# Optimization experiments

Hardware: AMD Instinct MI355X
Metric: run time of the kernel (lower is better)

The kernel has to match this reference:

```python
import jax, jax.numpy as jnp
import numpy as np

N_USERS = 50000
N0, N1, N2 = 200000, 50000, 12500
E0, E1, E2 = 1600000, 400000, 100000
B = 128
NUMP, TWEET, CATP, DES = 6, 768, 2, 768
IN_DIM, HID = 128, 128
SLOPE = 0.01  # LeakyReLU default


def setup_inputs() -> dict:
    key = jax.random.key(0)
    ks = iter(jax.random.split(key, 32))
    f32 = jnp.float32
    nrm = lambda s, sc=0.05: jax.random.normal(next(ks), s, f32) * sc
    inp = {}
    inp['x_raw'] = jax.random.normal(next(ks), (N_USERS, NUMP + TWEET + CATP + DES), f32)
    inp['W_des'] = nrm((DES, IN_DIM // 4)); inp['b_des'] = jnp.zeros((IN_DIM // 4,), f32)
    inp['W_tweet'] = nrm((TWEET, IN_DIM // 4)); inp['b_tweet'] = jnp.zeros((IN_DIM // 4,), f32)
    inp['W_num'] = nrm((NUMP, IN_DIM // 4)); inp['b_num'] = jnp.zeros((IN_DIM // 4,), f32)
    inp['W_cat'] = nrm((CATP, IN_DIM // 4)); inp['b_cat'] = jnp.zeros((IN_DIM // 4,), f32)
    inp['W_in'] = nrm((IN_DIM, HID)); inp['b_in'] = jnp.zeros((HID,), f32)
    inp['prelu_a'] = jnp.full((HID,), 0.25, f32)
    inp['W_conv'] = nrm((3, HID, HID)); inp['b_conv'] = jnp.zeros((3, HID), f32)
    inp['Wc1'] = nrm((3 * HID, HID)); inp['bc1'] = jnp.zeros((HID,), f32)
    inp['Wc2'] = nrm((HID, HID)); inp['bc2'] = jnp.zeros((HID,), f32)
    ri = lambda n, hi: jax.random.randint(next(ks), (n,), 0, hi, jnp.int32)
    inp['nodelist'] = ri(N0, N_USERS)
    inp['e0'] = jnp.stack([ri(E0, N0), ri(E0, N0)])
    inp['e1'] = jnp.stack([ri(E1, N1), ri(E1, N1)])
    inp['e2'] = jnp.stack([ri(E2, N2), ri(E2, N2)])
    inp['parent1'] = ri(N0, N1)   # coarsening assignment layer0 -> layer1
    inp['parent2'] = ri(N1, N2)   # layer1 -> layer2
    inp['batch1'] = jnp.sort(ri(N1, B))
    inp['batch2'] = jnp.sort(ri(N2, B))
    return inp


def _leaky(x):
    return jnp.where(x > 0, x, SLOPE * x)


def _gcn(h, ei, W, b, n):
    # GCNConv: lin -> sym-normalized add-aggregation with self-loops -> +bias
    h = h @ W
    loop = jnp.arange(n, dtype=ei.dtype)
    src = jnp.concatenate([ei[0], loop])
    dst = jnp.concatenate([ei[1], loop])
    deg = jax.ops.segment_sum(jnp.ones(dst.shape, h.dtype), dst, num_segments=n)
    dinv = jnp.where(deg > 0, jax.lax.rsqrt(deg), 0.0)
    msg = h[src] * (dinv[src] * dinv[dst])[:, None]
    return jax.ops.segment_sum(msg, dst, num_segments=n) + b


def reference(x_raw, W_des, b_des, W_tweet, b_tweet, W_num, b_num, W_cat, b_cat,
              W_in, b_in, prelu_a, W_conv, b_conv, Wc1, bc1, Wc2, bc2,
              nodelist, e0, e1, e2, parent1, parent2, batch1, batch2):
    # FeatureEncoder (twibot-20 slicing order: num_prop | tweet | cat_prop | des)
    n = _leaky(x_raw[:, :NUMP] @ W_num + b_num)
    t = _leaky(x_raw[:, NUMP:NUMP + TWEET] @ W_tweet + b_tweet)
    c = _leaky(x_raw[:, NUMP + TWEET:NUMP + TWEET + CATP] @ W_cat + b_cat)
    d = _leaky(x_raw[:, NUMP + TWEET + CATP:] @ W_des + b_des)
    h = jnp.concatenate([d, t, n, c], axis=1) @ W_in + b_in
    enc = jnp.where(h > 0, h, prelu_a * h)  # PReLU

    x = enc[nodelist]  # [N0, HID] gather per batched nodelists
    edges = [e0, e1, e2]
    sizes = [N0, N1, N2]
    parents = [parent1, parent2]
    nxt = [N1, N2]
    xs = []
    for i in range(3):
        x = jax.nn.relu(_gcn(x, edges[i], W_conv[i], b_conv[i], sizes[i]))
        if i < 2:  # SEPooling: pure scatter-add onto parent nodes (nn unused in its forward)
            x = jax.nn.relu(jax.ops.segment_sum(x, parents[i], num_segments=nxt[i]))
        xs.append(x)
    pooled = jnp.concatenate([
        jax.ops.segment_sum(xs[0], batch1, num_segments=B),
        jax.ops.segment_sum(xs[1], batch2, num_segments=B),
        jax.ops.segment_sum(xs[2], batch2, num_segments=B),
    ], axis=1)  # global sum pool, batch at layer min(i+1, tree_depth-1)
    z = jax.nn.relu(pooled @ Wc1 + bc1)  # dropout inactive (eval)
    return z @ Wc2 + bc2
```

## Files before the change

### kernel.cpp

```cpp
#include <hip/hip_runtime.h>

#define N_USERS 50000
#define NN0 200000
#define NN1 50000
#define NN2 12500
#define EE0 1600000
#define EE1 400000
#define EE2 100000

#define ENC_BLOCKS 782
#define CNT_BLOCKS 2295
#define GM2_BLOCKS 1563


__global__ __launch_bounds__(256) void k_enc_count(
    const float* __restrict__ xr,
    const float* __restrict__ Wd, const float* __restrict__ bd,
    const float* __restrict__ Wt, const float* __restrict__ bt,
    const float* __restrict__ Wn, const float* __restrict__ bn,
    const float* __restrict__ Wc, const float* __restrict__ bc,
    float* __restrict__ h128,
    const int* __restrict__ d0, const int* __restrict__ d1, const int* __restrict__ d2,
    const int* __restrict__ p1, const int* __restrict__ p2,
    int* __restrict__ degs, int* __restrict__ ranks)
{
    __shared__ float XsB[4368];
    __shared__ float Ws[32][68];
    __shared__ float xnc[64][8];
    __shared__ float Wl[8][64];

    if (blockIdx.x >= ENC_BLOCKS) {
        int t0 = (blockIdx.x - ENC_BLOCKS) * 256 + threadIdx.x;
        if (t0 >= 587500) return;
        #pragma unroll
        for (int k = 0; k < 4; k++) {
            int gid = t0 + k * 587500;
            int idx;
            if (gid < 1600000)      idx = d0[gid];
            else if (gid < 2000000) idx = 200704 + d1[gid - 1600000];
            else if (gid < 2100000) idx = 250880 + d2[gid - 2000000];
            else if (gid < 2300000) idx = 264192 + p1[gid - 2100000];
            else                    idx = 314368 + p2[gid - 2300000];
            ranks[gid] = atomicAdd(&degs[idx], 1);
        }
        return;
    }

    int t = threadIdx.x;
    int lane = t & 63, wv = t >> 6;
    int cg = t & 15, rg = t >> 4;
    int base = blockIdx.x * 64;

    if (t < 64) {
        int row = base + t;
        if (row < N_USERS) {
            const float* xp = xr + (size_t)row * 1544;
            float4 a = *(const float4*)xp;
            float2 b2 = *(const float2*)(xp + 4);
            float2 c2 = *(const float2*)(xp + 774);
            xnc[t][0] = a.x; xnc[t][1] = a.y; xnc[t][2] = a.z; xnc[t][3] = a.w;
            xnc[t][4] = b2.x; xnc[t][5] = b2.y; xnc[t][6] = c2.x; xnc[t][7] = c2.y;
        } else {
            #pragma unroll
            for (int k = 0; k < 8; k++) xnc[t][k] = 0.f;
        }
    } else if (t >= 192) {
        int l = t - 192;
        #pragma unroll
        for (int k = 0; k < 8; k++) {
            float w = 0.f;
            if (l < 32) { if (k < 6) w = Wn[k * 32 + l]; }
            else        { if (k >= 6) w = Wc[(k - 6) * 32 + (l - 32)]; }
            Wl[k][l] = w;
        }
    }

    int srow = (lane & 15) + wv * 16;
    int grow = base + srow;
    bool vrow = grow < N_USERS;
    const float* xrow = xr + (size_t)grow * 1544;

    float acc[4][4];
    #pragma unroll
    for (int r = 0; r < 4; r++)
        #pragma unroll
        for (int c = 0; c < 4; c++) acc[r][c] = 0.f;

    for (int kc = 0; kc < 768; kc += 32) {
        __syncthreads();
        #pragma unroll
        for (int h = 0; h < 2; h++) {
            int q = (lane >> 4) + h * 4;
            float4 vd = {0.f, 0.f, 0.f, 0.f};
            float2 va = {0.f, 0.f}, vb = {0.f, 0.f};
            if (vrow) {
                const float* xp = xrow + kc + q * 4;
                vd = *(const float4*)(xp + 776);
                va = *(const float2*)(xp + 6);
                vb = *(const float2*)(xp + 8);
            }
            int k0 = q * 4;
            XsB[(k0 + 0) * 68 + srow] = vd.x;
            XsB[(k0 + 1) * 68 + srow] = vd.y;
            XsB[(k0 + 2) * 68 + srow] = vd.z;
            XsB[(k0 + 3) * 68 + srow] = vd.w;
            XsB[2192 + (k0 + 0) * 68 + srow] = va.x;
            XsB[2192 + (k0 + 1) * 68 + srow] = va.y;
            XsB[2192 + (k0 + 2) * 68 + srow] = vb.x;
            XsB[2192 + (k0 + 3) * 68 + srow] = vb.y;
        }
        #pragma unroll
        for (int h = 0; h < 2; h++) {
            int fi = t + h * 256;
            int k = fi >> 4, c4 = (fi & 15) * 4;
            float4 w = (c4 < 32) ? *(const float4*)(Wd + (size_t)(kc + k) * 32 + c4)
                                 : *(const float4*)(Wt + (size_t)(kc + k) * 32 + (c4 - 32));
            *(float4*)&Ws[k][c4] = w;
        }
        __syncthreads();

        const float* Xp = (cg < 8) ? XsB : (XsB + 2192);
        #pragma unroll 8
        for (int k = 0; k < 32; k++) {
            float4 xv = *(const float4*)(Xp + k * 68 + rg * 4);
            float4 wv2 = *(const float4*)&Ws[k][cg * 4];
            acc[0][0] = fmaf(xv.x, wv2.x, acc[0][0]);
            acc[0][1] = fmaf(xv.x, wv2.y, acc[0][1]);
            acc[0][2] = fmaf(xv.x, wv2.z, acc[0][2]);
            acc[0][3] = fmaf(xv.x, wv2.w, acc[0][3]);
            acc[1][0] = fmaf(xv.y, wv2.x, acc[1][0]);
            acc[1][1] = fmaf(xv.y, wv2.y, acc[1][1]);
            acc[1][2] = fmaf(xv.y, wv2.z, acc[1][2]);
            acc[1][3] = fmaf(xv.y, wv2.w, acc[1][3]);
            acc[2][0] = fmaf(xv.z, wv2.x, acc[2][0]);
            acc[2][1] = fmaf(xv.z, wv2.y, acc[2][1]);
            acc[2][2] = fmaf(xv.z, wv2.z, acc[2][2]);
            acc[2][3] = fmaf(xv.z, wv2.w, acc[2][3]);
            acc[3][0] = fmaf(xv.w, wv2.x, acc[3][0]);
            acc[3][1] = fmaf(xv.w, wv2.y, acc[3][1]);
            acc[3][2] = fmaf(xv.w, wv2.z, acc[3][2]);
            acc[3][3] = fmaf(xv.w, wv2.w, acc[3][3]);
        }
    }

    float bh[4], bl[4], wlv[8][4];
    #pragma unroll
    for (int c = 0; c < 4; c++) {
        int j = cg * 4 + c;
        bh[c] = (j < 32) ? bd[j] : bt[j - 32];
        bl[c] = (j < 32) ? bn[j] : bc[j - 32];
        #pragma unroll
        for (int k = 0; k < 8; k++) wlv[k][c] = Wl[k][j];
    }
    #pragma unroll
    for (int r = 0; r < 4; r++) {
        int lr = rg * 4 + r;
        int row = base + lr;
        if (row >= N_USERS) break;
        float4 hv;
        float* ph = &hv.x;
        #pragma unroll
        for (int c = 0; c < 4; c++) {
            float v = acc[r][c] + bh[c];
            ph[c] = v > 0.f ? v : 0.01f * v;
        }
        *(float4*)(h128 + (size_t)row * 128 + cg * 4) = hv;
        float4 lv;
        float* pl = &lv.x;
        #pragma unroll
        for (int c = 0; c < 4; c++) {
            float v = bl[c];
            #pragma unroll
            for (int k = 0; k < 8; k++) v = fmaf(xnc[lr][k], wlv[k][c], v);
            pl[c] = v > 0.f ? v : 0.01f * v;
        }
        *(float4*)(h128 + (size_t)row * 128 + 64 + cg * 4) = lv;
    }
}

__global__ __launch_bounds__(256) void k_gemm2_scatter(
    const float* __restrict__ X, const float* __restrict__ W1,
    const float* __restrict__ b1, const float* __restrict__ pa,
    const float* __restrict__ W2, float* __restrict__ OUT, int n,
    const int* __restrict__ s0, const int* __restrict__ d0,
    const int* __restrict__ s1, const int* __restrict__ d1,
    const int* __restrict__ s2, const int* __restrict__ d2,
    const int* __restrict__ p1, const int* __restrict__ p2,
    const int* __restrict__ nl, const float* __restrict__ dinvs,
    const int* __restrict__ rowsts, const int* __restrict__ ranks,
    int* __restrict__ elists, float* __restrict__ edw)
{
    __shared__ float Xs[32][132];
    __shared__ float Wsh[32][132];

    if (blockIdx.x >= GM2_BLOCKS) {
        int t0 = (blockIdx.x - GM2_BLOCKS) * 256 + threadIdx.x;
        if (t0 >= 587500) return;
        #pragma unroll
        for (int k = 0; k < 4; k++) {
            int gid = t0 + k * 587500;
            if (gid < 1600000) {
                int s = s0[gid];
                int p = rowsts[d0[gid]] + ranks[gid];
                elists[p] = nl[s];
                edw[p] = dinvs[s];
            } else if (gid < 2000000) {
                int i = gid - 1600000;
                int s = s1[i];
                int p = rowsts[200704 + d1[i]] + ranks[gid];
                elists[1600000 + p] = s;
                edw[1600000 + p] = dinvs[200704 + s];
            } else if (gid < 2100000) {
                int i = gid - 2000000;
                int s = s2[i];
                int p = rowsts[250880 + d2[i]] + ranks[gid];
                elists[2000000 + p] = s;
                edw[2000000 + p] = dinvs[250880 + s];
            } else if (gid < 2300000) {
                int i = gid - 2100000;
                int p = rowsts[264192 + p1[i]] + ranks[gid];
                elists[2100000 + p] = i;
            } else {
                int i = gid - 2300000;
                int p = rowsts[314368 + p2[i]] + ranks[gid];
                elists[2300000 + p] = i;
            }
        }
        return;
    }

    int t = threadIdx.x;
    int cg = t & 31, rg = t >> 5;
    int base = blockIdx.x * 32;

    #pragma unroll
    for (int h = 0; h < 4; h++) {
        int fi = t + h * 256;
        int row = fi >> 5, q = fi & 31;
        float4 v = {0.f, 0.f, 0.f, 0.f};
        if (base + row < n) v = *(const float4*)(X + (size_t)(base + row) * 128 + q * 4);
        *(float4*)&Xs[row][q * 4] = v;
    }

    float acc[4][4];
    #pragma unroll
    for (int r = 0; r < 4; r++)
        #pragma unroll
        for (int c = 0; c < 4; c++) acc[r][c] = 0.f;

    for (int kc = 0; kc < 128; kc += 32) {
        __syncthreads();
        #pragma unroll
        for (int h = 0; h < 4; h++) {
            int fi = t + h * 256;
            int k = fi >> 5, q = fi & 31;
            *(float4*)&Wsh[k][q * 4] = *(const float4*)(W1 + (size_t)(kc + k) * 128 + q * 4);
        }
        __syncthreads();
        #pragma unroll
        for (int k4 = 0; k4 < 8; k4++) {
            int k = k4 * 4;
            float4 w0 = *(const float4*)&Wsh[k + 0][cg * 4];
            float4 w1 = *(const float4*)&Wsh[k + 1][cg * 4];
            float4 w2 = *(const float4*)&Wsh[k + 2][cg * 4];
            float4 w3 = *(const float4*)&Wsh[k + 3][cg * 4];
            #pragma unroll
            for (int r = 0; r < 4; r++) {
                float4 xv = *(const float4*)&Xs[rg * 4 + r][kc + k];
                acc[r][0] = fmaf(xv.w, w3.x, fmaf(xv.z, w2.x, fmaf(xv.y, w1.x, fmaf(xv.x, w0.x, acc[r][0]))));
                acc[r][1] = fmaf(xv.w, w3.y, fmaf(xv.z, w2.y, fmaf(xv.y, w1.y, fmaf(xv.x, w0.y, acc[r][1]))));
                acc[r][2] = fmaf(xv.w, w3.z, fmaf(xv.z, w2.z, fmaf(xv.y, w1.z, fmaf(xv.x, w0.z, acc[r][2]))));
                acc[r][3] = fmaf(xv.w, w3.w, fmaf(xv.z, w2.w, fmaf(xv.y, w1.w, fmaf(xv.x, w0.w, acc[r][3]))));
            }
        }
    }

    float4 bv = *(const float4*)(b1 + cg * 4);
    float4 pv = *(const float4*)(pa + cg * 4);
    __syncthreads();
    #pragma unroll
    for (int r = 0; r < 4; r++) {
        float v0 = acc[r][0] + bv.x; v0 = v0 > 0.f ? v0 : pv.x * v0;
        float v1 = acc[r][1] + bv.y; v1 = v1 > 0.f ? v1 : pv.y * v1;
        float v2 = acc[r][2] + bv.z; v2 = v2 > 0.f ? v2 : pv.z * v2;
        float v3 = acc[r][3] + bv.w; v3 = v3 > 0.f ? v3 : pv.w * v3;
        Xs[rg * 4 + r][cg * 4 + 0] = v0;
        Xs[rg * 4 + r][cg * 4 + 1] = v1;
        Xs[rg * 4 + r][cg * 4 + 2] = v2;
        Xs[rg * 4 + r][cg * 4 + 3] = v3;
        acc[r][0] = 0.f; acc[r][1] = 0.f; acc[r][2] = 0.f; acc[r][3] = 0.f;
    }

    for (int kc = 0; kc < 128; kc += 32) {
        __syncthreads();
        #pragma unroll
        for (int h = 0; h < 4; h++) {
            int fi = t + h * 256;
            int k = fi >> 5, q = fi & 31;
            *(float4*)&Wsh[k][q * 4] = *(const float4*)(W2 + (size_t)(kc + k) * 128 + q * 4);
        }
        __syncthreads();
        #pragma unroll
        for (int k4 = 0; k4 < 8; k4++) {
            int k = k4 * 4;
            float4 w0 = *(const float4*)&Wsh[k + 0][cg * 4];
            float4 w1 = *(const float4*)&Wsh[k + 1][cg * 4];
            float4 w2 = *(const float4*)&Wsh[k + 2][cg * 4];
            float4 w3 = *(const float4*)&Wsh[k + 3][cg * 4];
            #pragma unroll
            for (int r = 0; r < 4; r++) {
                float4 xv = *(const float4*)&Xs[rg * 4 + r][kc + k];
                acc[r][0] = fmaf(xv.w, w3.x, fmaf(xv.z, w2.x, fmaf(xv.y, w1.x, fmaf(xv.x, w0.x, acc[r][0]))));
                acc[r][1] = fmaf(xv.w, w3.y, fmaf(xv.z, w2.y, fmaf(xv.y, w1.y, fmaf(xv.x, w0.y, acc[r][1]))));
                acc[r][2] = fmaf(xv.w, w3.z, fmaf(xv.z, w2.z, fmaf(xv.y, w1.z, fmaf(xv.x, w0.z, acc[r][2]))));
                acc[r][3] = fmaf(xv.w, w3.w, fmaf(xv.z, w2.w, fmaf(xv.y, w1.w, fmaf(xv.x, w0.w, acc[r][3]))));
            }
        }
    }

    #pragma unroll
    for (int r = 0; r < 4; r++) {
        int row = base + rg * 4 + r;
        if (row >= n) break;
        float4 v;
        v.x = acc[r][0]; v.y = acc[r][1]; v.z = acc[r][2]; v.w = acc[r][3];
        *(float4*)(OUT + (size_t)row * 128 + cg * 4) = v;
    }
}

__global__ __launch_bounds__(256) void k_gemmT(
    const float* X, const float* __restrict__ W, float* OUT, int n)
{
    __shared__ float Xs[32][132];
    __shared__ float Ws[32][132];
    int t = threadIdx.x;
    int cg = t & 31, rg = t >> 5;
    int base = blockIdx.x * 32;

    #pragma unroll
    for (int h = 0; h < 4; h++) {
        int fi = t + h * 256;
        int row = fi >> 5, q = fi & 31;
        float4 v = {0.f, 0.f, 0.f, 0.f};
        if (base + row < n) v = *(const float4*)(X + (size_t)(base + row) * 128 + q * 4);
        *(float4*)&Xs[row][q * 4] = v;
    }

    float acc[4][4];
    #pragma unroll
    for (int r = 0; r < 4; r++)
        #pragma unroll
        for (int c = 0; c < 4; c++) acc[r][c] = 0.f;

    for (int kc = 0; kc < 128; kc += 32) {
        __syncthreads();
        #pragma unroll
        for (int h = 0; h < 4; h++) {
            int fi = t + h * 256;
            int k = fi >> 5, q = fi & 31;
            *(float4*)&Ws[k][q * 4] = *(const float4*)(W + (size_t)(kc + k) * 128 + q * 4);
        }
        __syncthreads();
        #pragma unroll
        for (int k4 = 0; k4 < 8; k4++) {
            int k = k4 * 4;
            float4 w0 = *(const float4*)&Ws[k + 0][cg * 4];
            float4 w1 = *(const float4*)&Ws[k + 1][cg * 4];
            float4 w2 = *(const float4*)&Ws[k + 2][cg * 4];
            float4 w3 = *(const float4*)&Ws[k + 3][cg * 4];
            #pragma unroll
            for (int r = 0; r < 4; r++) {
                float4 xv = *(const float4*)&Xs[rg * 4 + r][kc + k];
                acc[r][0] = fmaf(xv.w, w3.x, fmaf(xv.z, w2.x, fmaf(xv.y, w1.x, fmaf(xv.x, w0.x, acc[r][0]))));
                acc[r][1] = fmaf(xv.w, w3.y, fmaf(xv.z, w2.y, fmaf(xv.y, w1.y, fmaf(xv.x, w0.y, acc[r][1]))));
                acc[r][2] = fmaf(xv.w, w3.z, fmaf(xv.z, w2.z, fmaf(xv.y, w1.z, fmaf(xv.x, w0.z, acc[r][2]))));
                acc[r][3] = fmaf(xv.w, w3.w, fmaf(xv.z, w2.w, fmaf(xv.y, w1.w, fmaf(xv.x, w0.w, acc[r][3]))));
            }
        }
    }

    #pragma unroll
    for (int r = 0; r < 4; r++) {
        int row = base + rg * 4 + r;
        if (row >= n) break;
        float4 v;
        v.x = acc[r][0]; v.y = acc[r][1]; v.z = acc[r][2]; v.w = acc[r][3];
        *(float4*)(OUT + (size_t)row * 128 + cg * 4) = v;
    }
}

__device__ __forceinline__ void seg_of_scanblk(int b, int& doff, int& bsoff, int& lb) {
    if (b < 196)      { doff = 0;      bsoff = 0;   lb = b; }
    else if (b < 245) { doff = 200704; bsoff = 196; lb = b - 196; }
    else if (b < 258) { doff = 250880; bsoff = 245; lb = b - 245; }
    else if (b < 307) { doff = 264192; bsoff = 258; lb = b - 258; }
    else              { doff = 314368; bsoff = 307; lb = b - 307; }
}

__global__ __launch_bounds__(256) void k_scan_all(
    const int* __restrict__ degs, int* __restrict__ rowsts, int* __restrict__ bsums)
{
    __shared__ int sh[256];
    int doff, bsoff, lb;
    seg_of_scanblk(blockIdx.x, doff, bsoff, lb);
    int t = threadIdx.x;
    int base = doff + lb * 1024 + t * 4;
    int v[4], s = 0;
    #pragma unroll
    for (int k = 0; k < 4; k++) { v[k] = degs[base + k]; s += v[k]; }
    sh[t] = s;
    __syncthreads();
    for (int off = 1; off < 256; off <<= 1) {
        int x = 0;
        if (t >= off) x = sh[t - off];
        __syncthreads();
        if (t >= off) sh[t] += x;
        __syncthreads();
    }
    int ex = sh[t] - s;
    if (t == 255) bsums[bsoff + lb] = sh[255];
    #pragma unroll
    for (int k = 0; k < 4; k++) { rowsts[base + k] = ex; ex += v[k]; }
}

__global__ __launch_bounds__(256) void k_scanadd_all(
    int* __restrict__ rowsts, const int* __restrict__ bsums,
    const int* __restrict__ degs, float* __restrict__ dinvs)
{
    __shared__ int sh[256];
    int doff, bsoff, lb;
    seg_of_scanblk(blockIdx.x, doff, bsoff, lb);
    int t = threadIdx.x;
    sh[t] = (t < lb) ? bsums[bsoff + t] : 0;
    __syncthreads();
    #pragma unroll
    for (int off = 128; off >= 1; off >>= 1) {
        if (t < off) sh[t] += sh[t + off];
        __syncthreads();
    }
    int add = sh[0];
    int base = doff + lb * 1024 + t * 4;
    bool dodinv = (doff <= 250880);
    #pragma unroll
    for (int k = 0; k < 4; k++) {
        int i = base + k;
        rowsts[i] += add;
        if (dodinv) dinvs[i] = rsqrtf((float)degs[i] + 1.0f);
    }
}

__global__ __launch_bounds__(256) void k_gatherU_perm(
    const float* __restrict__ U, const int* __restrict__ nl,
    const int* __restrict__ rowst, const int* __restrict__ elist,
    const float* __restrict__ edw, const float* __restrict__ dinv,
    const float* __restrict__ bias, const int* __restrict__ perm,
    float* __restrict__ out, int n)
{
    size_t gid = (size_t)blockIdx.x * 256 + threadIdx.x;
    int i = (int)(gid >> 5);
    if (i >= n) return;
    int l = (int)(gid & 31);
    int d = perm[i];
    const float4* Uv = (const float4*)U;
    float dd = dinv[d];
    float4 self = Uv[(size_t)nl[d] * 32 + l];
    float4 acc;
    acc.x = self.x * dd; acc.y = self.y * dd; acc.z = self.z * dd; acc.w = self.w * dd;
    int s0 = rowst[d], s1 = rowst[d + 1];
    for (int e = s0; e < s1; ++e) {
        int srow = elist[e];
        float w = edw[e];
        float4 v = Uv[(size_t)srow * 32 + l];
        acc.x = fmaf(v.x, w, acc.x);
        acc.y = fmaf(v.y, w, acc.y);
        acc.z = fmaf(v.z, w, acc.z);
        acc.w = fmaf(v.w, w, acc.w);
    }
    const float4 b = ((const float4*)bias)[l];
    float4 y;
    y.x = fmaxf(fmaf(acc.x, dd, b.x), 0.f);
    y.y = fmaxf(fmaf(acc.y, dd, b.y), 0.f);
    y.z = fmaxf(fmaf(acc.z, dd, b.z), 0.f);
    y.w = fmaxf(fmaf(acc.w, dd, b.w), 0.f);
    ((float4*)out)[(size_t)i * 32 + l] = y;
}

__global__ __launch_bounds__(256) void k_gather_perm(
    const float* __restrict__ h, const int* __restrict__ rowst,
    const int* __restrict__ elist, const float* __restrict__ edw,
    const float* __restrict__ dinv, const float* __restrict__ bias,
    const int* __restrict__ perm, float* __restrict__ out, int n)
{
    size_t gid = (size_t)blockIdx.x * 256 + threadIdx.x;
    int i = (int)(gid >> 5);
    if (i >= n) return;
    int l = (int)(gid & 31);
    int d = perm ? perm[i] : i;
    const float4* hv = (const float4*)h;
    float dd = dinv[d];
    float4 self = hv[(size_t)d * 32 + l];
    float4 acc;
    acc.x = self.x * dd; acc.y = self.y * dd; acc.z = self.z * dd; acc.w = self.w * dd;
    int s0 = rowst[d], s1 = rowst[d + 1];
    for (int e = s0; e < s1; ++e) {
        int srow = elist[e];
        float w = edw[e];
        float4 v = hv[(size_t)srow * 32 + l];
        acc.x = fmaf(v.x, w, acc.x);
        acc.y = fmaf(v.y, w, acc.y);
        acc.z = fmaf(v.z, w, acc.z);
        acc.w = fmaf(v.w, w, acc.w);
    }
    const float4 b = ((const float4*)bias)[l];
    float4 y;
    y.x = fmaxf(fmaf(acc.x, dd, b.x), 0.f);
    y.y = fmaxf(fmaf(acc.y, dd, b.y), 0.f);
    y.z = fmaxf(fmaf(acc.z, dd, b.z), 0.f);
    y.w = fmaxf(fmaf(acc.w, dd, b.w), 0.f);
    ((float4*)out)[(size_t)i * 32 + l] = y;
}

__global__ __launch_bounds__(256) void k_poolseq(
    const float* __restrict__ Yp, const int* __restrict__ prowst,
    float* __restrict__ out, int np)
{
    size_t gid = (size_t)blockIdx.x * 256 + threadIdx.x;
    int p = (int)(gid >> 5);
    if (p >= np) return;
    int l = (int)(gid & 31);
    const float4* yv = (const float4*)Yp;
    float4 acc = {0.f, 0.f, 0.f, 0.f};
    int c0 = prowst[p], c1 = prowst[p + 1];
    for (int c = c0; c < c1; ++c) {
        float4 v = yv[(size_t)c * 32 + l];
        acc.x += v.x; acc.y += v.y; acc.z += v.z; acc.w += v.w;
    }
    float4 y;
    y.x = fmaxf(acc.x, 0.f); y.y = fmaxf(acc.y, 0.f);
    y.z = fmaxf(acc.z, 0.f); y.w = fmaxf(acc.w, 0.f);
    ((float4*)out)[(size_t)p * 32 + l] = y;
}

__global__ __launch_bounds__(128) void k_bpool_all(
    const float* __restrict__ X1, const float* __restrict__ X2, const float* __restrict__ Y2,
    const int* __restrict__ b1, const int* __restrict__ b2, float* __restrict__ pl)
{
    int b = blockIdx.x;
    const float* src; const int* bidx; int coloff, n, r0;
    if (b < 391)      { src = X1; bidx = b1; coloff = 0;   n = 50000; r0 = b * 128; }
    else if (b < 489) { src = X2; bidx = b2; coloff = 128; n = 12500; r0 = (b - 391) * 128; }
    else              { src = Y2; bidx = b2; coloff = 256; n = 12500; r0 = (b - 489) * 128; }
    if (r0 >= n) return;
    int j = threadIdx.x;
    int r1 = min(r0 + 128, n);
    float acc = 0.f;
    int prev = bidx[r0];
    for (int r = r0; r < r1; ++r) {
        int bb = bidx[r];
        if (bb != prev) {
            unsafeAtomicAdd(&pl[(size_t)prev * 384 + coloff + j], acc);
            acc = 0.f; prev = bb;
        }
        acc += src[(size_t)r * 128 + j];
    }
    unsafeAtomicAdd(&pl[(size_t)prev * 384 + coloff + j], acc);
}

__global__ void k_mlp2(const float* __restrict__ PL,
                       const float* __restrict__ Wc1, const float* __restrict__ bc1,
                       const float* __restrict__ Wc2, const float* __restrict__ bc2,
                       float* __restrict__ out)
{
    __shared__ float as[384];
    __shared__ float zs[128];
    int r = blockIdx.x, j = threadIdx.x;
    as[j] = PL[(size_t)r * 384 + j];
    as[j + 128] = PL[(size_t)r * 384 + 128 + j];
    as[j + 256] = PL[(size_t)r * 384 + 256 + j];
    __syncthreads();
    float acc = bc1[j];
    for (int k = 0; k < 384; k++) acc = fmaf(as[k], Wc1[(size_t)k * 128 + j], acc);
    zs[j] = fmaxf(acc, 0.f);
    __syncthreads();
    float o = bc2[j];
    for (int k = 0; k < 128; k++) o = fmaf(zs[k], Wc2[(size_t)k * 128 + j], o);
    out[(size_t)r * 128 + j] = o;
}

extern "C" void kernel_launch(void* const* d_in, const int* in_sizes, int n_in,
                              void* d_out, int out_size, void* d_ws, size_t ws_size,
                              hipStream_t stream)
{
    const float* x_raw  = (const float*)d_in[0];
    const float* W_des  = (const float*)d_in[1];
    const float* b_des  = (const float*)d_in[2];
    const float* W_twe  = (const float*)d_in[3];
    const float* b_twe  = (const float*)d_in[4];
    const float* W_num  = (const float*)d_in[5];
    const float* b_num  = (const float*)d_in[6];
    const float* W_cat  = (const float*)d_in[7];
    const float* b_cat  = (const float*)d_in[8];
    const float* W_in   = (const float*)d_in[9];
    const float* b_in   = (const float*)d_in[10];
    const float* prelua = (const float*)d_in[11];
    const float* W_conv = (const float*)d_in[12];
    const float* b_conv = (const float*)d_in[13];
    const float* Wc1    = (const float*)d_in[14];
    const float* bc1    = (const float*)d_in[15];
    const float* Wc2    = (const float*)d_in[16];
    const float* bc2    = (const float*)d_in[17];
    const int* nodelist = (const int*)d_in[18];
    const int* e0       = (const int*)d_in[19];
    const int* e1       = (const int*)d_in[20];
    const int* e2       = (const int*)d_in[21];
    const int* parent1  = (const int*)d_in[22];
    const int* parent2  = (const int*)d_in[23];
    const int* batch1   = (const int*)d_in[24];
    const int* batch2   = (const int*)d_in[25];

    float* WS  = (float*)d_ws;
    float* ENC = WS;
    float* U   = WS + 6400000;
    float* H   = WS + 12800000;
    float* Y   = WS + 19200000;
    float* X1  = WS + 44800000;
    float* X2  = WS + 51200000;
    float* PL  = WS + 52800000;
    float* EDW = WS + 52900000;
    int*   DEGS   = (int*)(WS + 55000000);
    int*   ROWSTS = DEGS + 327680;
    float* DINVS  = (float*)(ROWSTS + 327680);
    int*   BSUMS  = (int*)(DINVS + 264192);
    int*   RANKS  = BSUMS + 512;
    int*   ELISTS = RANKS + 2350000;

    hipMemsetAsync(PL, 0, (size_t)128 * 384 * 4, stream);
    hipMemsetAsync(DEGS, 0, (size_t)327680 * 4, stream);

    k_enc_count<<<ENC_BLOCKS + CNT_BLOCKS, 256, 0, stream>>>(
        x_raw, W_des, b_des, W_twe, b_twe, W_num, b_num, W_cat, b_cat, ENC,
        e0 + EE0, e1 + EE1, e2 + EE2, parent1, parent2, DEGS, RANKS);

    k_scan_all<<<320, 256, 0, stream>>>(DEGS, ROWSTS, BSUMS);
    k_scanadd_all<<<320, 256, 0, stream>>>(ROWSTS, BSUMS, DEGS, DINVS);

    k_gemm2_scatter<<<GM2_BLOCKS + CNT_BLOCKS, 256, 0, stream>>>(
        ENC, W_in, b_in, prelua, W_conv, U, N_USERS,
        e0, e0 + EE0, e1, e1 + EE1, e2, e2 + EE2, parent1, parent2,
        nodelist, DINVS, ROWSTS, RANKS, ELISTS, EDW);

    k_gatherU_perm<<<(int)(((size_t)NN0 * 32 + 255) / 256), 256, 0, stream>>>(
        U, nodelist, ROWSTS, ELISTS, EDW, DINVS, b_conv,
        ELISTS + 2100000, Y, NN0);
    k_poolseq<<<(int)(((size_t)NN1 * 32 + 255) / 256), 256, 0, stream>>>(
        Y, ROWSTS + 264192, X1, NN1);

    k_gemmT<<<(NN1 + 31) / 32, 256, 0, stream>>>(X1, W_conv + 16384, H, NN1);
    k_gather_perm<<<(int)(((size_t)NN1 * 32 + 255) / 256), 256, 0, stream>>>(
        H, ROWSTS + 200704, ELISTS + 1600000, EDW + 1600000, DINVS + 200704,
        b_conv + 128, ELISTS + 2300000, Y, NN1);
    k_poolseq<<<(int)(((size_t)NN2 * 32 + 255) / 256), 256, 0, stream>>>(
        Y, ROWSTS + 314368, X2, NN2);

    k_gemmT<<<(NN2 + 31) / 32, 256, 0, stream>>>(X2, W_conv + 32768, H, NN2);
    k_gather_perm<<<(int)(((size_t)NN2 * 32 + 255) / 256), 256, 0, stream>>>(
        H, ROWSTS + 250880, ELISTS + 2000000, EDW + 2000000, DINVS + 250880,
        b_conv + 256, nullptr, Y, NN2);

    k_bpool_all<<<587, 128, 0, stream>>>(X1, X2, Y, batch1, batch2, PL);

    k_mlp2<<<128, 128, 0, stream>>>(PL, Wc1, bc1, Wc2, bc2, (float*)d_out);
}
```

Before: 646.9 us.

## Split encoder K-dimension across two block sets and defer bias/activation to consumer

The encoder GEMM's 768-long reduction is split in half across two sets of blocks, doubling the block count from 782 to 1564 for better occupancy of the MI355X's CUs. Each half writes a partial sum to a separate buffer (enc0 and enc1, with enc1 aliased onto H). The following gemm2 kernel then sums the partials, adds the biases, and applies LeakyReLU while loading its tile. This costs an extra 64-column write and read of partial sums per row, plus a bias staging sync.

```diff
diff --git a/kernel.cpp b/kernel.cpp
--- a/kernel.cpp
+++ b/kernel.cpp
@@ -8,18 +8,17 @@
 #define EE1 400000
 #define EE2 100000
 
-#define ENC_BLOCKS 782
+#define ENC_SPLIT_BLOCKS 782
+#define ENC_TOT 1564
 #define CNT_BLOCKS 2295
 #define GM2_BLOCKS 1563
 
 
 __global__ __launch_bounds__(256) void k_enc_count(
     const float* __restrict__ xr,
-    const float* __restrict__ Wd, const float* __restrict__ bd,
-    const float* __restrict__ Wt, const float* __restrict__ bt,
-    const float* __restrict__ Wn, const float* __restrict__ bn,
-    const float* __restrict__ Wc, const float* __restrict__ bc,
-    float* __restrict__ h128,
+    const float* __restrict__ Wd, const float* __restrict__ Wt,
+    const float* __restrict__ Wn, const float* __restrict__ Wc,
+    float* __restrict__ enc0, float* __restrict__ enc1,
     const int* __restrict__ d0, const int* __restrict__ d1, const int* __restrict__ d2,
     const int* __restrict__ p1, const int* __restrict__ p2,
     int* __restrict__ degs, int* __restrict__ ranks)
@@ -29,8 +28,8 @@
     __shared__ float xnc[64][8];
     __shared__ float Wl[8][64];
 
-    if (blockIdx.x >= ENC_BLOCKS) {
-        int t0 = (blockIdx.x - ENC_BLOCKS) * 256 + threadIdx.x;
+    if (blockIdx.x >= ENC_TOT) {
+        int t0 = (blockIdx.x - ENC_TOT) * 256 + threadIdx.x;
         if (t0 >= 587500) return;
         #pragma unroll
         for (int k = 0; k < 4; k++) {
@@ -46,32 +45,37 @@
         return;
     }
 
+    int split = (blockIdx.x >= ENC_SPLIT_BLOCKS) ? 1 : 0;
+    int blk = blockIdx.x - split * ENC_SPLIT_BLOCKS;
+    int kc0 = split * 384;
     int t = threadIdx.x;
     int lane = t & 63, wv = t >> 6;
     int cg = t & 15, rg = t >> 4;
-    int base = blockIdx.x * 64;
-
-    if (t < 64) {
-        int row = base + t;
-        if (row < N_USERS) {
-            const float* xp = xr + (size_t)row * 1544;
-            float4 a = *(const float4*)xp;
-            float2 b2 = *(const float2*)(xp + 4);
-            float2 c2 = *(const float2*)(xp + 774);
-            xnc[t][0] = a.x; xnc[t][1] = a.y; xnc[t][2] = a.z; xnc[t][3] = a.w;
-            xnc[t][4] = b2.x; xnc[t][5] = b2.y; xnc[t][6] = c2.x; xnc[t][7] = c2.y;
-        } else {
+    int base = blk * 64;
+
+    if (split == 0) {
+        if (t < 64) {
+            int row = base + t;
+            if (row < N_USERS) {
+                const float* xp = xr + (size_t)row * 1544;
+                float4 a = *(const float4*)xp;
+                float2 b2 = *(const float2*)(xp + 4);
+                float2 c2 = *(const float2*)(xp + 774);
+                xnc[t][0] = a.x; xnc[t][1] = a.y; xnc[t][2] = a.z; xnc[t][3] = a.w;
+                xnc[t][4] = b2.x; xnc[t][5] = b2.y; xnc[t][6] = c2.x; xnc[t][7] = c2.y;
+            } else {
+                #pragma unroll
+                for (int k = 0; k < 8; k++) xnc[t][k] = 0.f;
+            }
+        } else if (t >= 192) {
+            int l = t - 192;
             #pragma unroll
-            for (int k = 0; k < 8; k++) xnc[t][k] = 0.f;
-        }
-    } else if (t >= 192) {
-        int l = t - 192;
-        #pragma unroll
-        for (int k = 0; k < 8; k++) {
-            float w = 0.f;
-            if (l < 32) { if (k < 6) w = Wn[k * 32 + l]; }
-            else        { if (k >= 6) w = Wc[(k - 6) * 32 + (l - 32)]; }
-            Wl[k][l] = w;
+            for (int k = 0; k < 8; k++) {
+                float w = 0.f;
+                if (l < 32) { if (k < 6) w = Wn[k * 32 + l]; }
+                else        { if (k >= 6) w = Wc[(k - 6) * 32 + (l - 32)]; }
+                Wl[k][l] = w;
+            }
         }
     }
 
@@ -86,7 +90,8 @@
         #pragma unroll
         for (int c = 0; c < 4; c++) acc[r][c] = 0.f;
 
-    for (int kc = 0; kc < 768; kc += 32) {
+    for (int kk = 0; kk < 384; kk += 32) {
+        int kc = kc0 + kk;
         __syncthreads();
         #pragma unroll
         for (int h = 0; h < 2; h++) {
@@ -143,45 +148,50 @@
         }
     }
 
-    float bh[4], bl[4], wlv[8][4];
-    #pragma unroll
-    for (int c = 0; c < 4; c++) {
-        int j = cg * 4 + c;
-        bh[c] = (j < 32) ? bd[j] : bt[j - 32];
-        bl[c] = (j < 32) ? bn[j] : bc[j - 32];
-        #pragma unroll
-        for (int k = 0; k < 8; k++) wlv[k][c] = Wl[k][j];
-    }
-    #pragma unroll
-    for (int r = 0; r < 4; r++) {
-        int lr = rg * 4 + r;
-        int row = base + lr;
-        if (row >= N_USERS) break;
-        float4 hv;
-        float* ph = &hv.x;
-        #pragma unroll
-        for (int c = 0; c < 4; c++) {
-            float v = acc[r][c] + bh[c];
-            ph[c] = v > 0.f ? v : 0.01f * v;
-        }
-        *(float4*)(h128 + (size_t)row * 128 + cg * 4) = hv;
-        float4 lv;
-        float* pl = &lv.x;
-        #pragma unroll
-        for (int c = 0; c < 4; c++) {
-            float v = bl[c];
+    if (split == 0) {
+        float wlv[8][4];
+        #pragma unroll
+        for (int c = 0; c < 4; c++)
             #pragma unroll
-            for (int k = 0; k < 8; k++) v = fmaf(xnc[lr][k], wlv[k][c], v);
-            pl[c] = v > 0.f ? v : 0.01f * v;
-        }
-        *(float4*)(h128 + (size_t)row * 128 + 64 + cg * 4) = lv;
+            for (int k = 0; k < 8; k++) wlv[k][c] = Wl[k][cg * 4 + c];
+        #pragma unroll
+        for (int r = 0; r < 4; r++) {
+            int lr = rg * 4 + r;
+            int row = base + lr;
+            if (row >= N_USERS) break;
+            float4 hv;
+            hv.x = acc[r][0]; hv.y = acc[r][1]; hv.z = acc[r][2]; hv.w = acc[r][3];
+            *(float4*)(enc0 + (size_t)row * 128 + cg * 4) = hv;
+            float4 lv;
+            float* pl = &lv.x;
+            #pragma unroll
+            for (int c = 0; c < 4; c++) {
+                float v = 0.f;
+                #pragma unroll
+                for (int k = 0; k < 8; k++) v = fmaf(xnc[lr][k], wlv[k][c], v);
+                pl[c] = v;
+            }
+            *(float4*)(enc0 + (size_t)row * 128 + 64 + cg * 4) = lv;
+        }
+    } else {
+        #pragma unroll
+        for (int r = 0; r < 4; r++) {
+            int row = base + rg * 4 + r;
+            if (row >= N_USERS) break;
+            float4 hv;
+            hv.x = acc[r][0]; hv.y = acc[r][1]; hv.z = acc[r][2]; hv.w = acc[r][3];
+            *(float4*)(enc1 + (size_t)row * 64 + cg * 4) = hv;
+        }
     }
 }
 
 __global__ __launch_bounds__(256) void k_gemm2_scatter(
-    const float* __restrict__ X, const float* __restrict__ W1,
-    const float* __restrict__ b1, const float* __restrict__ pa,
-    const float* __restrict__ W2, float* __restrict__ OUT, int n,
+    const float* __restrict__ enc0, const float* __restrict__ enc1,
+    const float* __restrict__ bd, const float* __restrict__ bt,
+    const float* __restrict__ bn, const float* __restrict__ bc,
+    const float* __restrict__ W1, const float* __restrict__ b1,
+    const float* __restrict__ pa, const float* __restrict__ W2,
+    float* __restrict__ OUT, int n,
     const int* __restrict__ s0, const int* __restrict__ d0,
     const int* __restrict__ s1, const int* __restrict__ d1,
     const int* __restrict__ s2, const int* __restrict__ d2,
@@ -192,6 +202,7 @@
 {
     __shared__ float Xs[32][132];
     __shared__ float Wsh[32][132];
+    __shared__ float bsh[128];
 
     if (blockIdx.x >= GM2_BLOCKS) {
         int t0 = (blockIdx.x - GM2_BLOCKS) * 256 + threadIdx.x;
@@ -233,12 +244,29 @@
     int cg = t & 31, rg = t >> 5;
     int base = blockIdx.x * 32;
 
+    if (t < 128)
+        bsh[t] = (t < 32) ? bd[t] : (t < 64) ? bt[t - 32]
+               : (t < 96) ? bn[t - 64] : bc[t - 96];
+    __syncthreads();
+
     #pragma unroll
     for (int h = 0; h < 4; h++) {
         int fi = t + h * 256;
         int row = fi >> 5, q = fi & 31;
         float4 v = {0.f, 0.f, 0.f, 0.f};
-        if (base + row < n) v = *(const float4*)(X + (size_t)(base + row) * 128 + q * 4);
+        if (base + row < n) {
+            v = *(const float4*)(enc0 + (size_t)(base + row) * 128 + q * 4);
+            if (q < 16) {
+                float4 e1 = *(const float4*)(enc1 + (size_t)(base + row) * 64 + q * 4);
+                v.x += e1.x; v.y += e1.y; v.z += e1.z; v.w += e1.w;
+            }
+            v.x += bsh[q * 4 + 0]; v.y += bsh[q * 4 + 1];
+            v.z += bsh[q * 4 + 2]; v.w += bsh[q * 4 + 3];
+            v.x = v.x > 0.f ? v.x : 0.01f * v.x;
+            v.y = v.y > 0.f ? v.y : 0.01f * v.y;
+            v.z = v.z > 0.f ? v.z : 0.01f * v.z;
+            v.w = v.w > 0.f ? v.w : 0.01f * v.w;
+        }
         *(float4*)&Xs[row][q * 4] = v;
     }
 
@@ -618,15 +646,16 @@
     const int* batch1   = (const int*)d_in[24];
     const int* batch2   = (const int*)d_in[25];
 
-    float* WS  = (float*)d_ws;
-    float* ENC = WS;
-    float* U   = WS + 6400000;
-    float* H   = WS + 12800000;
-    float* Y   = WS + 19200000;
-    float* X1  = WS + 44800000;
-    float* X2  = WS + 51200000;
-    float* PL  = WS + 52800000;
-    float* EDW = WS + 52900000;
+    float* WS   = (float*)d_ws;
+    float* ENC0 = WS;
+    float* U    = WS + 6400000;
+    float* H    = WS + 12800000;
+    float* ENC1 = H;
+    float* Y    = WS + 19200000;
+    float* X1   = WS + 44800000;
+    float* X2   = WS + 51200000;
+    float* PL   = WS + 52800000;
+    float* EDW  = WS + 52900000;
     int*   DEGS   = (int*)(WS + 55000000);
     int*   ROWSTS = DEGS + 327680;
     float* DINVS  = (float*)(ROWSTS + 327680);
@@ -637,15 +666,16 @@
     hipMemsetAsync(PL, 0, (size_t)128 * 384 * 4, stream);
     hipMemsetAsync(DEGS, 0, (size_t)327680 * 4, stream);
 
-    k_enc_count<<<ENC_BLOCKS + CNT_BLOCKS, 256, 0, stream>>>(
-        x_raw, W_des, b_des, W_twe, b_twe, W_num, b_num, W_cat, b_cat, ENC,
+    k_enc_count<<<ENC_TOT + CNT_BLOCKS, 256, 0, stream>>>(
+        x_raw, W_des, W_twe, W_num, W_cat, ENC0, ENC1,
         e0 + EE0, e1 + EE1, e2 + EE2, parent1, parent2, DEGS, RANKS);
 
     k_scan_all<<<320, 256, 0, stream>>>(DEGS, ROWSTS, BSUMS);
     k_scanadd_all<<<320, 256, 0, stream>>>(ROWSTS, BSUMS, DEGS, DINVS);
 
     k_gemm2_scatter<<<GM2_BLOCKS + CNT_BLOCKS, 256, 0, stream>>>(
-        ENC, W_in, b_in, prelua, W_conv, U, N_USERS,
+        ENC0, ENC1, b_des, b_twe, b_num, b_cat,
+        W_in, b_in, prelua, W_conv, U, N_USERS,
         e0, e0 + EE0, e1, e1 + EE1, e2, e2 + EE2, parent1, parent2,
         nodelist, DINVS, ROWSTS, RANKS, ELISTS, EDW);
 
```

Result: slower. 678.7 us (+4.9%).
